# Performance work log

Hardware: AMD Instinct MI355X
Metric: run time of the kernel (lower is better)

Reference implementation:

```python
import jax, jax.numpy as jnp
import numpy as np

NUM_HEADS = 8
NUM_HYPEREDGES = 64
NODE_DIM = 512
HEAD_DIM = NODE_DIM // NUM_HEADS
SCALING = float(np.sqrt(HEAD_DIM))


def setup_inputs() -> dict:
    key = jax.random.key(0)
    ks = jax.random.split(key, 6)
    B, N, D, M = 16, 4096, NODE_DIM, NUM_HYPEREDGES
    X = jax.random.normal(ks[0], (B, N, D), dtype=jnp.float32)
    # xavier_uniform for prototype_base [M, D]
    lim_p = float(np.sqrt(6.0 / (M + D)))
    prototype_base = jax.random.uniform(ks[1], (M, D), minval=-lim_p, maxval=lim_p, dtype=jnp.float32)
    # context_net: Linear(2D -> M*D), torch default init ~ U(-1/sqrt(fan_in), ...)
    lim_c = 1.0 / float(np.sqrt(2 * D))
    W_ctx = jax.random.uniform(ks[2], (M * D, 2 * D), minval=-lim_c, maxval=lim_c, dtype=jnp.float32)
    b_ctx = jax.random.uniform(ks[3], (M * D,), minval=-lim_c, maxval=lim_c, dtype=jnp.float32)
    # pre_head_proj: Linear(D -> D)
    lim_h = 1.0 / float(np.sqrt(D))
    W_pre = jax.random.uniform(ks[4], (D, D), minval=-lim_h, maxval=lim_h, dtype=jnp.float32)
    b_pre = jax.random.uniform(ks[5], (D,), minval=-lim_h, maxval=lim_h, dtype=jnp.float32)
    return {"X": X, "prototype_base": prototype_base, "W_ctx": W_ctx, "b_ctx": b_ctx,
            "W_pre": W_pre, "b_pre": b_pre}


def reference(X, prototype_base, W_ctx, b_ctx, W_pre, b_pre):
    B, N, D = X.shape
    M, H, hd = NUM_HYPEREDGES, NUM_HEADS, HEAD_DIM
    # context pooling: mean + max over nodes -> [B, 2D]
    ctx = jnp.concatenate([X.mean(axis=1), X.max(axis=1)], axis=-1)
    # per-batch prototype offsets: [B, M, D]
    offsets = (ctx @ W_ctx.T + b_ctx).reshape(B, M, D)
    prototypes = prototype_base[None, :, :] + offsets  # [B, M, D]
    # project nodes
    X_proj = X @ W_pre.T + b_pre  # [B, N, D]
    Xh = X_proj.reshape(B, N, H, hd)       # [B, N, H, hd]
    Ph = prototypes.reshape(B, M, H, hd)   # [B, M, H, hd]
    # per-head attention logits, mean over heads: [B, N, M]
    logits = jnp.einsum('bnhd,bmhd->bnm', Xh, Ph) / (SCALING * H)
    # dropout is identity in eval mode; softmax over the NODE axis (dim=1)
    return jax.nn.softmax(logits, axis=1)
```

## Files before the change

### kernel.cpp

```cpp
#include <hip/hip_runtime.h>
#include <math.h>

#define B_ 16
#define N_ 4096
#define D_ 512
#define M_ 64
#define MD 32768

typedef __attribute__((ext_vector_type(4))) float f32x4;
typedef __attribute__((ext_vector_type(8))) short short8;

#define OFF_PSUM   0
#define OFF_PMAXP  1048576
#define OFF_CTXB   2097152
#define OFF_PB     2105344
#define OFF_WPT    2367488
#define OFF_CB     2498560
#define OFF_GMAX   2499584
#define OFF_GINV   2500608
#define OFF_TPMAX  2501632
#define OFF_TPSUM  2763776
#define OFF_QB     3025920
#define OFF_LGB    3288064

__device__ __forceinline__ unsigned short f2bf(float f) {
    unsigned int u = __float_as_uint(f);
    u += 0x7fffu + ((u >> 16) & 1u);
    return (unsigned short)(u >> 16);
}
__device__ __forceinline__ float bf2f(unsigned short u) {
    return __uint_as_float(((unsigned int)u) << 16);
}

__global__ __launch_bounds__(256) void k_pool(const float* __restrict__ X, float* __restrict__ ws) {
    int b = blockIdx.x >> 6, nc = blockIdx.x & 63, t = threadIdx.x;
    int c = t & 127, p = t >> 7;
    const float4* X4 = (const float4*)X;
    float4 s = make_float4(0.f, 0.f, 0.f, 0.f);
    float4 mx = make_float4(-INFINITY, -INFINITY, -INFINITY, -INFINITY);
    int rowbase = b * N_ + nc * 64 + p;
#pragma unroll 8
    for (int i = 0; i < 32; i++) {
        int n = rowbase + 2 * i;
        float4 v = X4[n * 128 + c];
        s.x += v.x; s.y += v.y; s.z += v.z; s.w += v.w;
        mx.x = fmaxf(mx.x, v.x); mx.y = fmaxf(mx.y, v.y);
        mx.z = fmaxf(mx.z, v.z); mx.w = fmaxf(mx.w, v.w);
    }
    int slot = (b * 128 + nc * 2 + p) * 128 + c;
    ((float4*)(ws + OFF_PSUM))[slot] = s;
    ((float4*)(ws + OFF_PMAXP))[slot] = mx;
}

__global__ __launch_bounds__(256) void k_prep(const float* __restrict__ Wp, float* __restrict__ ws) {
    __shared__ __align__(16) char smem[8448];
    int bx = blockIdx.x, t = threadIdx.x;
    if (bx < 64) {
        f32x4* red = (f32x4*)smem;
        int b = bx >> 2, q = bx & 3;
        int lane = t & 63, w = t >> 6;
        bool isMax = (q >= 2);
        const f32x4* SRC = (const f32x4*)(ws + (isMax ? OFF_PMAXP : OFF_PSUM));
        int kk = (q & 1) * 64 + lane;
        f32x4 acc;
        if (isMax) acc = (f32x4){-INFINITY, -INFINITY, -INFINITY, -INFINITY};
        else       acc = (f32x4){0.f, 0.f, 0.f, 0.f};
#pragma unroll 8
        for (int i = 0; i < 32; i++) {
            int c = w * 32 + i;
            f32x4 v = SRC[(b * 128 + c) * 128 + kk];
            if (isMax) {
                acc[0] = fmaxf(acc[0], v[0]); acc[1] = fmaxf(acc[1], v[1]);
                acc[2] = fmaxf(acc[2], v[2]); acc[3] = fmaxf(acc[3], v[3]);
            } else {
                acc[0] += v[0]; acc[1] += v[1]; acc[2] += v[2]; acc[3] += v[3];
            }
        }
        red[t] = acc;
        __syncthreads();
        if (t < 64) {
            f32x4 a = red[t], b1 = red[64 + t], c1 = red[128 + t], d = red[192 + t];
            f32x4 r;
            if (isMax) {
#pragma unroll
                for (int j = 0; j < 4; j++) r[j] = fmaxf(fmaxf(a[j], b1[j]), fmaxf(c1[j], d[j]));
            } else {
#pragma unroll
                for (int j = 0; j < 4; j++) r[j] = (a[j] + b1[j] + c1[j] + d[j]) * (1.0f / 4096.0f);
            }
            ushort4 o;
            o.x = f2bf(r[0]); o.y = f2bf(r[1]); o.z = f2bf(r[2]); o.w = f2bf(r[3]);
            ((ushort4*)(ws + OFF_CTXB))[b * 256 + q * 64 + t] = o;
        }
    } else {
        unsigned short (*lt)[65] = (unsigned short(*)[65])smem;
        int bb = bx - 64;
        int ti = bb >> 3, tj = bb & 7;
        int sub = t >> 6, lane = t & 63;
#pragma unroll
        for (int i = 0; i < 16; i++) {
            int dl = i * 4 + sub;
            int jl = lane;
            lt[jl][dl] = f2bf(Wp[(ti * 64 + dl) * 512 + tj * 64 + jl]);
        }
        __syncthreads();
        unsigned short* WT = (unsigned short*)(ws + OFF_WPT);
#pragma unroll
        for (int i = 0; i < 16; i++) {
            int jl = i * 4 + sub;
            int dl = lane;
            WT[(tj * 64 + jl) * 512 + ti * 64 + dl] = lt[jl][dl];
        }
    }
}

__global__ __launch_bounds__(256) void k_protos(const float* __restrict__ Wc, const float* __restrict__ pb,
                                                const float* __restrict__ bc, float* __restrict__ ws) {
    int t = threadIdx.x;
    int wave = blockIdx.x * 4 + (t >> 6);
    int l = t & 63;
    int r0 = wave * 16;
    int row = r0 + (l & 15);
    int kg = l >> 4;
    const f32x4* W4 = (const f32x4*)Wc;
    const short8* CB8 = (const short8*)(ws + OFF_CTXB);
    f32x4 acc = (f32x4){0.f, 0.f, 0.f, 0.f};
    int wb = row * 256 + kg * 2;
    int cbase = (l & 15) * 128 + kg;
#pragma unroll 8
    for (int kc = 0; kc < 32; kc++) {
        f32x4 xa = __builtin_nontemporal_load(W4 + wb + kc * 8);
        f32x4 xb = __builtin_nontemporal_load(W4 + wb + kc * 8 + 1);
        short8 wf;
        wf[0] = (short)f2bf(xa[0]); wf[1] = (short)f2bf(xa[1]);
        wf[2] = (short)f2bf(xa[2]); wf[3] = (short)f2bf(xa[3]);
        wf[4] = (short)f2bf(xb[0]); wf[5] = (short)f2bf(xb[1]);
        wf[6] = (short)f2bf(xb[2]); wf[7] = (short)f2bf(xb[3]);
        short8 cf = CB8[cbase + kc * 4];
        acc = __builtin_amdgcn_mfma_f32_16x16x32_bf16(cf, wf, acc, 0, 0, 0);
    }
    int r = r0 + (l & 15);
    float add = pb[r] + bc[r];
    unsigned short* Pb = (unsigned short*)(ws + OFF_PB);
#pragma unroll
    for (int i = 0; i < 4; i++) {
        int bb = kg * 4 + i;
        Pb[bb * MD + r] = f2bf(acc[i] + add);
    }
}

__global__ __launch_bounds__(256) void k_q(const float* __restrict__ bpre, float* __restrict__ ws) {
    int t = threadIdx.x;
    int b = blockIdx.x >> 5, ctile = blockIdx.x & 31;
    int mt = t >> 6, l = t & 63;
    int col = l & 15, kg = l >> 4;
    const short8* WT8 = (const short8*)((const unsigned short*)(ws + OFF_WPT));
    const short8* Pb8 = (const short8*)((const unsigned short*)(ws + OFF_PB));
    f32x4 acc = (f32x4){0.f, 0.f, 0.f, 0.f};
    int abase = (ctile * 16 + col) * 64 + kg;
    int bbase = (b * 64 + mt * 16 + col) * 64 + kg;
#pragma unroll 4
    for (int kc = 0; kc < 16; kc++) {
        short8 af = WT8[abase + kc * 4];
        short8 bf = Pb8[bbase + kc * 4];
        acc = __builtin_amdgcn_mfma_f32_16x16x32_bf16(af, bf, acc, 0, 0, 0);
    }
    union { unsigned short u[4]; uint2 v; } pk;
#pragma unroll
    for (int i = 0; i < 4; i++) pk.u[i] = f2bf(acc[i] * (1.0f / 64.0f));
    int g = (ctile & 1) * 2 + (kg >> 1);
    int fidx = b * 4096 + ((ctile >> 1) * 4 + mt) * 64 + g * 16 + col;
    ((uint2*)((unsigned short*)(ws + OFF_QB)))[fidx * 2 + (kg & 1)] = pk.v;

    if (blockIdx.x < 256) {
        int w = blockIdx.x * 4 + (t >> 6);
        int bb = w >> 6, mm = w & 63;
        const short8* P2 = (const short8*)((const unsigned short*)(ws + OFF_PB) + bb * MD + mm * 512);
        short8 p = P2[l];
        const float4* bp4 = (const float4*)bpre;
        float4 q0 = bp4[l * 2], q1 = bp4[l * 2 + 1];
        float s = bf2f((unsigned short)p[0]) * q0.x + bf2f((unsigned short)p[1]) * q0.y
                + bf2f((unsigned short)p[2]) * q0.z + bf2f((unsigned short)p[3]) * q0.w
                + bf2f((unsigned short)p[4]) * q1.x + bf2f((unsigned short)p[5]) * q1.y
                + bf2f((unsigned short)p[6]) * q1.z + bf2f((unsigned short)p[7]) * q1.w;
#pragma unroll
        for (int off = 1; off < 64; off <<= 1) s += __shfl_xor(s, off);
        if (l == 0) ws[OFF_CB + w] = s * (1.0f / 64.0f);
    }
}

__global__ __launch_bounds__(256) void k_logits(const float* __restrict__ X, float* __restrict__ ws) {
    int t = threadIdx.x;
    int W = blockIdx.x * 4 + (t >> 6);
    int b = W >> 8, nt = W & 255;
    int l = t & 63, col = l & 15, kg = l >> 4;
    int nA = nt * 16 + col;
    const float4* X4 = (const float4*)X;
    const short8* Qb8 = (const short8*)((const unsigned short*)(ws + OFF_QB));
    f32x4 acc[4];
#pragma unroll
    for (int mt = 0; mt < 4; mt++) acc[mt] = (f32x4){0.f, 0.f, 0.f, 0.f};

    int xbase4 = ((b * N_ + nA) * D_) >> 2;
    int qfrag = b * 4096 + l;

    float4 pxa[8], pxb[8];
#pragma unroll
    for (int i = 0; i < 8; i++) {
        pxa[i] = X4[xbase4 + i * 8 + kg * 2];
        pxb[i] = X4[xbase4 + i * 8 + kg * 2 + 1];
    }
#pragma unroll
    for (int kc = 0; kc < 16; kc++) {
        float4 xa = pxa[kc & 7];
        float4 xb = pxb[kc & 7];
        if (kc < 8) {
            pxa[kc & 7] = X4[xbase4 + (kc + 8) * 8 + kg * 2];
            pxb[kc & 7] = X4[xbase4 + (kc + 8) * 8 + kg * 2 + 1];
        }
        short8 af;
        af[0] = (short)f2bf(xa.x); af[1] = (short)f2bf(xa.y);
        af[2] = (short)f2bf(xa.z); af[3] = (short)f2bf(xa.w);
        af[4] = (short)f2bf(xb.x); af[5] = (short)f2bf(xb.y);
        af[6] = (short)f2bf(xb.z); af[7] = (short)f2bf(xb.w);
#pragma unroll
        for (int mt = 0; mt < 4; mt++) {
            short8 bfr = Qb8[qfrag + (kc * 4 + mt) * 64];
            acc[mt] = __builtin_amdgcn_mfma_f32_16x16x32_bf16(af, bfr, acc[mt], 0, 0, 0);
        }
    }
    const float* cb = ws + OFF_CB + b * 64;
    unsigned short* LGB = (unsigned short*)(ws + OFF_LGB) + b * (N_ * 64) + nt * 16 * 64;
#pragma unroll
    for (int mt = 0; mt < 4; mt++) {
        int m = mt * 16 + col;
        float c = cb[m];
        float v0 = acc[mt][0] + c, v1 = acc[mt][1] + c;
        float v2 = acc[mt][2] + c, v3 = acc[mt][3] + c;
        int nr = kg * 4;
        LGB[(nr + 0) * 64 + m] = f2bf(v0);
        LGB[(nr + 1) * 64 + m] = f2bf(v1);
        LGB[(nr + 2) * 64 + m] = f2bf(v2);
        LGB[(nr + 3) * 64 + m] = f2bf(v3);
        float mx = fmaxf(fmaxf(v0, v1), fmaxf(v2, v3));
        mx = fmaxf(mx, __shfl_xor(mx, 16));
        mx = fmaxf(mx, __shfl_xor(mx, 32));
        float s = expf(v0 - mx) + expf(v1 - mx) + expf(v2 - mx) + expf(v3 - mx);
        s += __shfl_xor(s, 16);
        s += __shfl_xor(s, 32);
        if (kg == 0) {
            ws[OFF_TPMAX + (b * 64 + m) * 256 + nt] = mx;
            ws[OFF_TPSUM + (b * 64 + m) * 256 + nt] = s;
        }
    }
}

__global__ __launch_bounds__(256) void k_combine(float* __restrict__ ws) {
    int t = threadIdx.x;
    int w = blockIdx.x * 4 + (t >> 6);
    int l = t & 63;
    float4 a  = ((const float4*)(ws + OFF_TPMAX + w * 256))[l];
    float4 s4 = ((const float4*)(ws + OFF_TPSUM + w * 256))[l];
    float g = fmaxf(fmaxf(a.x, a.y), fmaxf(a.z, a.w));
    float s = s4.x * expf(a.x - g) + s4.y * expf(a.y - g)
            + s4.z * expf(a.z - g) + s4.w * expf(a.w - g);
#pragma unroll
    for (int off = 1; off < 64; off <<= 1) {
        float og = __shfl_xor(g, off);
        float os = __shfl_xor(s, off);
        float ng = fmaxf(g, og);
        s = s * expf(g - ng) + os * expf(og - ng);
        g = ng;
    }
    if (l == 0) { ws[OFF_GMAX + w] = g; ws[OFF_GINV + w] = 1.0f / s; }
}

__global__ __launch_bounds__(256) void k_final(const float* __restrict__ ws, float* __restrict__ out) {
    int idx = blockIdx.x * 256 + threadIdx.x;
    int flat = idx * 8;
    int b = flat >> 18;
    int m0 = flat & 63;
    uint4 lg = ((const uint4*)((const unsigned short*)(ws + OFF_LGB)))[idx];
    int bm = b * 64 + m0;
    float4 ga = *(const float4*)(ws + OFF_GMAX + bm);
    float4 gb = *(const float4*)(ws + OFF_GMAX + bm + 4);
    float4 ia = *(const float4*)(ws + OFF_GINV + bm);
    float4 ib = *(const float4*)(ws + OFF_GINV + bm + 4);
    float4 o0, o1;
    o0.x = expf(__uint_as_float(lg.x << 16)         - ga.x) * ia.x;
    o0.y = expf(__uint_as_float(lg.x & 0xffff0000u) - ga.y) * ia.y;
    o0.z = expf(__uint_as_float(lg.y << 16)         - ga.z) * ia.z;
    o0.w = expf(__uint_as_float(lg.y & 0xffff0000u) - ga.w) * ia.w;
    o1.x = expf(__uint_as_float(lg.z << 16)         - gb.x) * ib.x;
    o1.y = expf(__uint_as_float(lg.z & 0xffff0000u) - gb.y) * ib.y;
    o1.z = expf(__uint_as_float(lg.w << 16)         - gb.z) * ib.z;
    o1.w = expf(__uint_as_float(lg.w & 0xffff0000u) - gb.w) * ib.w;
    ((float4*)out)[idx * 2]     = o0;
    ((float4*)out)[idx * 2 + 1] = o1;
}

extern "C" void kernel_launch(void* const* d_in, const int* in_sizes, int n_in,
                              void* d_out, int out_size, void* d_ws, size_t ws_size,
                              hipStream_t stream) {
    const float* X  = (const float*)d_in[0];
    const float* pb = (const float*)d_in[1];
    const float* Wc = (const float*)d_in[2];
    const float* bc = (const float*)d_in[3];
    const float* Wp = (const float*)d_in[4];
    const float* bp = (const float*)d_in[5];
    float* ws  = (float*)d_ws;
    float* out = (float*)d_out;

    k_pool<<<1024, 256, 0, stream>>>(X, ws);
    k_prep<<<128, 256, 0, stream>>>(Wp, ws);
    k_protos<<<512, 256, 0, stream>>>(Wc, pb, bc, ws);
    k_q<<<512, 256, 0, stream>>>(bp, ws);
    k_logits<<<1024, 256, 0, stream>>>(X, ws);
    k_combine<<<256, 256, 0, stream>>>(ws);
    k_final<<<2048, 256, 0, stream>>>(ws, out);
}
```

Before: 119.0 us.

## Stage X tile as bf16 in swizzled LDS and split M across waves

The logits kernel now loads a 32-row X tile per block with fully coalesced float4 reads, converts it to bf16 once and stores it in shared memory with an XOR swizzle. Each of four waves then reads its MFMA A-fragments from LDS and computes two of the four M tiles, so the grid doubles to 2048 blocks. The aim is better global-load coalescing and more parallelism than the old strided per-lane X reads with register prefetch. In exchange it adds a block barrier and 32KB of LDS per block, which may limit occupancy.

Result: no change. 117.7 us, median of 2 (-1.1%).

```diff
diff --git a/kernel.cpp b/kernel.cpp
--- a/kernel.cpp
+++ b/kernel.cpp
@@ -190,53 +190,52 @@
 }
 
 __global__ __launch_bounds__(256) void k_logits(const float* __restrict__ X, float* __restrict__ ws) {
+    __shared__ unsigned short xls[16384];
     int t = threadIdx.x;
-    int W = blockIdx.x * 4 + (t >> 6);
-    int b = W >> 8, nt = W & 255;
-    int l = t & 63, col = l & 15, kg = l >> 4;
-    int nA = nt * 16 + col;
+    int b = blockIdx.x >> 7, ntp = blockIdx.x & 127;
+
     const float4* X4 = (const float4*)X;
+    int xrowbase = (b * N_ + ntp * 32) * 128;
+#pragma unroll
+    for (int j = 0; j < 16; j++) {
+        int flat = j * 256 + t;
+        int row = flat >> 7, qc = flat & 127;
+        float4 v = X4[xrowbase + row * 128 + qc];
+        ushort4 o;
+        o.x = f2bf(v.x); o.y = f2bf(v.y); o.z = f2bf(v.z); o.w = f2bf(v.w);
+        int byte = (row << 10) + ((qc << 3) ^ ((row & 7) << 4));
+        *(ushort4*)((char*)xls + byte) = o;
+    }
+    __syncthreads();
+
+    int w = t >> 6, l = t & 63, col = l & 15, kg = l >> 4;
+    int ntl = w & 1;
+    int nt = ntp * 2 + ntl;
+    int mt0 = (w >> 1) * 2;
     const short8* Qb8 = (const short8*)((const unsigned short*)(ws + OFF_QB));
-    f32x4 acc[4];
-#pragma unroll
-    for (int mt = 0; mt < 4; mt++) acc[mt] = (f32x4){0.f, 0.f, 0.f, 0.f};
-
-    int xbase4 = ((b * N_ + nA) * D_) >> 2;
     int qfrag = b * 4096 + l;
-
-    float4 pxa[8], pxb[8];
-#pragma unroll
-    for (int i = 0; i < 8; i++) {
-        pxa[i] = X4[xbase4 + i * 8 + kg * 2];
-        pxb[i] = X4[xbase4 + i * 8 + kg * 2 + 1];
-    }
+    f32x4 acc[2];
+    acc[0] = (f32x4){0.f, 0.f, 0.f, 0.f};
+    acc[1] = (f32x4){0.f, 0.f, 0.f, 0.f};
+    int rl = ntl * 16 + col;
+    int rhi = rl << 10, rx = (rl & 7) << 4;
 #pragma unroll
     for (int kc = 0; kc < 16; kc++) {
-        float4 xa = pxa[kc & 7];
-        float4 xb = pxb[kc & 7];
-        if (kc < 8) {
-            pxa[kc & 7] = X4[xbase4 + (kc + 8) * 8 + kg * 2];
-            pxb[kc & 7] = X4[xbase4 + (kc + 8) * 8 + kg * 2 + 1];
-        }
-        short8 af;
-        af[0] = (short)f2bf(xa.x); af[1] = (short)f2bf(xa.y);
-        af[2] = (short)f2bf(xa.z); af[3] = (short)f2bf(xa.w);
-        af[4] = (short)f2bf(xb.x); af[5] = (short)f2bf(xb.y);
-        af[6] = (short)f2bf(xb.z); af[7] = (short)f2bf(xb.w);
-#pragma unroll
-        for (int mt = 0; mt < 4; mt++) {
-            short8 bfr = Qb8[qfrag + (kc * 4 + mt) * 64];
-            acc[mt] = __builtin_amdgcn_mfma_f32_16x16x32_bf16(af, bfr, acc[mt], 0, 0, 0);
+        short8 af = *(const short8*)((const char*)xls + rhi + (((kc << 6) + (kg << 4)) ^ rx));
+#pragma unroll
+        for (int mi = 0; mi < 2; mi++) {
+            short8 bfr = Qb8[qfrag + (kc * 4 + mt0 + mi) * 64];
+            acc[mi] = __builtin_amdgcn_mfma_f32_16x16x32_bf16(af, bfr, acc[mi], 0, 0, 0);
         }
     }
     const float* cb = ws + OFF_CB + b * 64;
     unsigned short* LGB = (unsigned short*)(ws + OFF_LGB) + b * (N_ * 64) + nt * 16 * 64;
 #pragma unroll
-    for (int mt = 0; mt < 4; mt++) {
-        int m = mt * 16 + col;
+    for (int mi = 0; mi < 2; mi++) {
+        int m = (mt0 + mi) * 16 + col;
         float c = cb[m];
-        float v0 = acc[mt][0] + c, v1 = acc[mt][1] + c;
-        float v2 = acc[mt][2] + c, v3 = acc[mt][3] + c;
+        float v0 = acc[mi][0] + c, v1 = acc[mi][1] + c;
+        float v2 = acc[mi][2] + c, v3 = acc[mi][3] + c;
         int nr = kg * 4;
         LGB[(nr + 0) * 64 + m] = f2bf(v0);
         LGB[(nr + 1) * 64 + m] = f2bf(v1);
@@ -315,7 +314,7 @@
     k_prep<<<128, 256, 0, stream>>>(Wp, ws);
     k_protos<<<512, 256, 0, stream>>>(Wc, pb, bc, ws);
     k_q<<<512, 256, 0, stream>>>(bp, ws);
-    k_logits<<<1024, 256, 0, stream>>>(X, ws);
+    k_logits<<<2048, 256, 0, stream>>>(X, ws);
     k_combine<<<256, 256, 0, stream>>>(ws);
     k_final<<<2048, 256, 0, stream>>>(ws, out);
 }
```
